# Optimization experiments

Hardware: AMD Instinct MI355X
Metric: run time of the kernel (lower is better)

Reference implementation:

```python
import jax, jax.numpy as jnp
import numpy as np

H, W, C = 512, 512, 21
D_BI, D_SP = 5, 2
THETA_ALPHA, THETA_BETA, THETA_GAMMA = 80.0, 13.0, 3.0
BILATERAL_COMPAT, SPATIAL_COMPAT, COMPAT = 10.0, 3.0, -1.0
NUM_ITER = 5


def _build_lattice(feats):
    # Permutohedral lattice construction (Adams et al. 2010), vectorized numpy.
    # feats: [N, d] float64 -> (offsets [N,d+1] int32 into M lattice points,
    # barycentric weights [N,d+1] float32, blur_neighbors [d+1, M, 2] int32 (+1, 0=missing)).
    N, d = feats.shape
    scale = (np.sqrt(2.0 / 3.0) * (d + 1)) / np.sqrt((np.arange(d) + 1.0) * (np.arange(d) + 2.0))
    cf = feats * scale                                            # [N, d]
    S = np.concatenate([np.cumsum(cf[:, ::-1], axis=1)[:, ::-1], np.zeros((N, 1))], axis=1)
    elev = np.empty((N, d + 1))
    elev[:, 0] = S[:, 0]
    elev[:, 1:] = S[:, 1:] - np.arange(1, d + 1) * cf             # embed on H_d hyperplane
    rem0 = np.floor(elev / (d + 1) + 0.5) * (d + 1)               # nearest 0-colored point
    sums = np.rint(rem0.sum(1) / (d + 1)).astype(np.int64)
    diff = elev - rem0
    idx = np.arange(d + 1)
    gt = diff[:, None, :] > diff[:, :, None]
    eq = (diff[:, None, :] == diff[:, :, None]) & (idx[None, None, :] < idx[None, :, None])
    rank = (gt | eq).sum(2).astype(np.int64) + sums[:, None]
    lo = rank < 0
    rank += (d + 1) * lo
    rem0 += (d + 1) * lo
    hi = rank > d
    rank -= (d + 1) * hi
    rem0 -= (d + 1) * hi
    v = (elev - rem0) / (d + 1)
    b = np.zeros((N, d + 2))
    rows = np.arange(N)[:, None]
    np.add.at(b, (rows, d - rank), v)
    np.add.at(b, (rows, d + 1 - rank), -v)
    b[:, 0] += 1.0 + b[:, d + 1]
    ws = b[:, :d + 1].astype(np.float32)                          # weight per remainder r
    rem0i = np.rint(rem0[:, :d]).astype(np.int64)
    r = np.arange(d + 1)
    keys = rem0i[:, None, :] + r[None, :, None] - (d + 1) * (rank[:, None, :d] > (d - r)[None, :, None])
    uniq, os_flat = np.unique(keys.reshape(-1, d), axis=0, return_inverse=True)
    M = uniq.shape[0]
    os_ = os_flat.reshape(N, d + 1).astype(np.int32)
    n1 = np.repeat(uniq[None] + 1, d + 1, axis=0)                 # [d+1, M, d]
    n2 = np.repeat(uniq[None] - 1, d + 1, axis=0)
    for j in range(d):
        n1[j, :, j] = uniq[:, j] - d
        n2[j, :, j] = uniq[:, j] + d
    allk = np.concatenate([uniq, n1.reshape(-1, d), n2.reshape(-1, d)], axis=0)
    _, inv = np.unique(allk, axis=0, return_inverse=True)
    lut = np.full(int(inv.max()) + 1, -1, np.int64)
    lut[inv[:M]] = np.arange(M)
    i1 = lut[inv[M:M + (d + 1) * M]].reshape(d + 1, M)
    i2 = lut[inv[M + (d + 1) * M:]].reshape(d + 1, M)
    bn = (np.stack([i1, i2], axis=-1) + 1).astype(np.int32)       # 0 == missing neighbor
    return os_, ws, bn


def setup_inputs():
    key = jax.random.key(0)
    k1, k2 = jax.random.split(key)
    unary = jax.random.normal(k1, (H, W, C), jnp.float32)
    # piecewise-constant random image (realistic local color coherence)
    base = np.asarray(jax.random.uniform(k2, (32, 32, 3)), dtype=np.float64) * 255.0
    image = np.kron(base, np.ones((H // 32, W // 32, 1)))
    yy, xx = np.mgrid[0:H, 0:W].astype(np.float64)
    bi = np.concatenate([np.stack([xx / THETA_ALPHA, yy / THETA_ALPHA], -1),
                         image / THETA_BETA], axis=-1).reshape(-1, D_BI)
    sp = np.stack([xx / THETA_GAMMA, yy / THETA_GAMMA], -1).reshape(-1, D_SP)
    os_b, ws_b, bn_b = _build_lattice(bi)
    os_s, ws_s, bn_s = _build_lattice(sp)
    return {'unary': unary,
            'ws_b': jnp.asarray(ws_b), 'ws_s': jnp.asarray(ws_s),
            'os_b': jnp.asarray(os_b), 'os_s': jnp.asarray(os_s),
            'bn_b': jnp.asarray(bn_b), 'bn_s': jnp.asarray(bn_s)}


def _filter(Q, os_, ws, bn, alpha):
    # splat -> blur -> slice over one permutohedral lattice
    M = bn.shape[1]
    vals = jnp.zeros((M + 1, Q.shape[-1]), Q.dtype)
    vals = vals.at[os_ + 1].add(ws[:, :, None] * Q[:, None, :])   # splat (row 0 = pad)
    for j in range(bn.shape[0]):                                  # blur along d+1 lattice axes
        vals = vals.at[1:].add(0.5 * (vals[bn[j, :, 0]] + vals[bn[j, :, 1]]))
    return alpha * jnp.einsum('nj,njc->nc', ws, vals[os_ + 1])    # slice


def reference(unary, ws_b, ws_s, os_b, os_s, bn_b, bn_s):
    U = unary.reshape(-1, unary.shape[-1])                        # [N, C]
    a_b = 1.0 / (1.0 + 2.0 ** (-D_BI))
    a_s = 1.0 / (1.0 + 2.0 ** (-D_SP))
    ones = jnp.ones((U.shape[0], 1), U.dtype)
    inv_nb = 1.0 / (_filter(ones, os_b, ws_b, bn_b, a_b) + 1e-20)
    inv_ns = 1.0 / (_filter(ones, os_s, ws_s, bn_s, a_s) + 1e-20)
    Q = jax.nn.softmax(-U, axis=-1)
    for _ in range(NUM_ITER):
        msg = BILATERAL_COMPAT * (_filter(Q, os_b, ws_b, bn_b, a_b) * inv_nb) \
            + SPATIAL_COMPAT * (_filter(Q, os_s, ws_s, bn_s, a_s) * inv_ns)
        Q = jax.nn.softmax(-U - COMPAT * msg, axis=-1)
    return Q.reshape(unary.shape)
```

## Files before the change

### kernel.cpp

```cpp
#include <hip/hip_runtime.h>
#include <hip/hip_fp16.h>

#define NCH 21
#define NCH2 22
#define VSH 32
#define QSH 32
#define USH 24
#define NPIX (512*512)
#define DECODE12 (1.0f/(4095.f*128.f))
#define DECODE14 (1.0f/(16383.f*128.f))

__device__ __forceinline__ float2 bits2f2(float b) {
  __half2 h = __builtin_bit_cast(__half2, b);
  return __half22float2(h);
}
__device__ __forceinline__ float f22bits(float x, float y) {
  __half2 h = __floats2half2_rn(x, y);
  return __builtin_bit_cast(float, h);
}

__device__ __forceinline__ int wave_rank_atomic(int m, bool valid, int* __restrict__ cur) {
  int lane = threadIdx.x & 63;
  unsigned long long todo = __ballot(valid);
  int out = 0;
  while (todo) {
    int leader = __ffsll((unsigned long long)todo) - 1;
    int lm = __shfl(m, leader);
    unsigned long long match = __ballot(valid && (m == lm));
    int cnt = __popcll(match);
    int b = 0;
    if (lane == leader) b = atomicAdd(&cur[lm], cnt);
    b = __shfl(b, leader);
    if (valid && (m == lm)) out = b + __popcll(match & ((1ull << lane) - 1ull));
    todo &= ~match;
  }
  return out;
}


__global__ void pack_count_kernel(const int* __restrict__ os_b, const float* __restrict__ ws_b,
                                  const int* __restrict__ os_s, const float* __restrict__ ws_s,
                                  unsigned int* __restrict__ sl, int* __restrict__ cnt,
                                  int nptot, int Mb) {
  int t = blockIdx.x*blockDim.x + threadIdx.x;
  bool valid = (t < nptot);
  int m = 0; float w = 0.f;
  if (valid) {
    if (t < 6*NPIX) { int j = t >> 18, n = t & (NPIX-1); m = os_b[n*6+j]; w = ws_b[n*6+j]; }
    else { int t2 = t - 6*NPIX; int j = t2 >> 18, n = t2 & (NPIX-1);
           m = Mb + os_s[n*3+j]; w = ws_s[n*3+j]; }
    int w12 = (int)(w * 4095.f + 0.5f);
    w12 = w12 < 0 ? 0 : (w12 > 4095 ? 4095 : w12);
    sl[t] = ((unsigned int)(m+1) << 12) | (unsigned int)w12;
  }
  int lane = threadIdx.x & 63;
  unsigned long long todo = __ballot(valid);
  while (todo) {
    int leader = __ffsll((unsigned long long)todo) - 1;
    int lm = __shfl(m, leader);
    unsigned long long match = __ballot(valid && (m == lm));
    if (lane == leader) atomicAdd(&cnt[lm], __popcll(match));
    todo &= ~match;
  }
}

__global__ void count_fused_kernel(const int* __restrict__ os_b, const int* __restrict__ os_s,
                                   int* __restrict__ cnt, int nptot, int Mb) {
  int t = blockIdx.x*blockDim.x + threadIdx.x;
  bool valid = (t < nptot);
  int m = 0;
  if (valid) {
    if (t < 6*NPIX) { int j = t >> 18, n = t & (NPIX-1); m = os_b[n*6+j]; }
    else { int t2 = t - 6*NPIX; int j = t2 >> 18, n = t2 & (NPIX-1); m = Mb + os_s[n*3+j]; }
  }
  int lane = threadIdx.x & 63;
  unsigned long long todo = __ballot(valid);
  while (todo) {
    int leader = __ffsll((unsigned long long)todo) - 1;
    int lm = __shfl(m, leader);
    unsigned long long match = __ballot(valid && (m == lm));
    if (lane == leader) atomicAdd(&cnt[lm], __popcll(match));
    todo &= ~match;
  }
}

__global__ void scan_block_kernel(const int* __restrict__ cnt, int* __restrict__ excl,
                                  int* __restrict__ bsum, int M) {
  __shared__ int s[256];
  int i = blockIdx.x*256 + threadIdx.x;
  int v = (i < M) ? cnt[i] : 0;
  s[threadIdx.x] = v;
  __syncthreads();
  for (int off = 1; off < 256; off <<= 1) {
    int t = (threadIdx.x >= off) ? s[threadIdx.x - off] : 0;
    __syncthreads();
    s[threadIdx.x] += t;
    __syncthreads();
  }
  if (i < M) excl[i] = s[threadIdx.x] - v;
  if (threadIdx.x == 255) bsum[blockIdx.x] = s[255];
}

__global__ void scan_sums_kernel(int* __restrict__ bsum, int nb) {
  __shared__ int s[256];
  __shared__ int carry;
  if (threadIdx.x == 0) carry = 0;
  __syncthreads();
  for (int base = 0; base < nb; base += 256) {
    int i = base + threadIdx.x;
    int v = (i < nb) ? bsum[i] : 0;
    s[threadIdx.x] = v;
    __syncthreads();
    for (int off = 1; off < 256; off <<= 1) {
      int t = (threadIdx.x >= off) ? s[threadIdx.x - off] : 0;
      __syncthreads();
      s[threadIdx.x] += t;
      __syncthreads();
    }
    if (i < nb) bsum[i] = s[threadIdx.x] - v + carry;
    int tot = s[255];
    __syncthreads();
    if (threadIdx.x == 0) carry += tot;
    __syncthreads();
  }
  if (threadIdx.x == 0) bsum[nb] = carry;
}

__global__ void scan_add_kernel(int* __restrict__ excl, const int* __restrict__ bsum,
                                int M, int nb) {
  int i = blockIdx.x*blockDim.x + threadIdx.x;
  if (i < M) excl[i] += bsum[i >> 8];
  else if (i == M) excl[M] = bsum[nb];
}

__global__ void fill_packed_kernel(const unsigned int* __restrict__ sl,
                                   const int* __restrict__ start, int* __restrict__ cur,
                                   unsigned int* __restrict__ pw, int nptot) {
  int t = blockIdx.x*blockDim.x + threadIdx.x;
  bool valid = (t < nptot);
  int m = 0; unsigned int e = 0;
  if (valid) {
    e = sl[t];
    m = (int)(e >> 12) - 1;
  }
  int slot = wave_rank_atomic(m, valid, cur);
  if (valid) {
    unsigned int pix = (unsigned int)(t & (NPIX-1));
    pw[start[m] + slot] = (pix << 12) | (e & 4095u);
  }
}

__global__ void fill_fused_kernel(const int* __restrict__ os_b, const float* __restrict__ ws_b,
                                  const int* __restrict__ os_s, const float* __restrict__ ws_s,
                                  const int* __restrict__ start, int* __restrict__ cur,
                                  unsigned int* __restrict__ pw, int nptot, int Mb) {
  int t = blockIdx.x*blockDim.x + threadIdx.x;
  bool valid = (t < nptot);
  int m = 0, pix = 0; float w = 0.f;
  if (valid) {
    if (t < 6*NPIX) { int j = t >> 18, n = t & (NPIX-1); m = os_b[n*6+j]; pix = n; w = ws_b[n*6+j]; }
    else { int t2 = t - 6*NPIX; int j = t2 >> 18, n = t2 & (NPIX-1);
           m = Mb + os_s[n*3+j]; pix = n; w = ws_s[n*3+j]; }
  }
  int slot = wave_rank_atomic(m, valid, cur);
  if (valid) {
    int w14 = (int)(w * 16383.f + 0.5f);
    w14 = w14 < 0 ? 0 : (w14 > 16383 ? 16383 : w14);
    pw[start[m] + slot] = ((unsigned int)pix << 14) | (unsigned int)w14;
  }
}


__global__ void gather_half2_kernel(const __half* __restrict__ Qh, const int* __restrict__ start,
                                    const unsigned int* __restrict__ pw,
                                    __half* __restrict__ valsB, __half* __restrict__ valsS,
                                    int Mb, int Mtot) {
  int wid = blockIdx.x*(blockDim.x >> 6) + (threadIdx.x >> 6);
  if (wid >= Mtot) return;
  int lane = threadIdx.x & 63;
  int pg = lane/11;
  int c2 = lane - pg*11;
  int k0 = start[wid], k1 = start[wid+1];
  float ax = 0.f, ay = 0.f, wsum = 0.f;
  if (pg < 5) {
    int k = k0 + pg;
    for (; k + 5 < k1; k += 10) {
      unsigned int e0 = pw[k], e1 = pw[k+5];
      float w0 = (float)(e0 & 4095u), w1 = (float)(e1 & 4095u);
      float2 f0 = __half22float2(*(const __half2*)(Qh + ((size_t)(e0 >> 12) << 5) + 2*c2));
      float2 f1 = __half22float2(*(const __half2*)(Qh + ((size_t)(e1 >> 12) << 5) + 2*c2));
      ax += w0*f0.x + w1*f1.x;
      ay += w0*f0.y + w1*f1.y;
      wsum += w0 + w1;
    }
    if (k < k1) {
      unsigned int e0 = pw[k];
      float w0 = (float)(e0 & 4095u);
      float2 f0 = __half22float2(*(const __half2*)(Qh + ((size_t)(e0 >> 12) << 5) + 2*c2));
      ax += w0*f0.x; ay += w0*f0.y; wsum += w0;
    }
  }
  float sx = ax, sy = ay, wt = wsum;
  #pragma unroll
  for (int g = 1; g < 5; ++g) {
    sx += __shfl(ax, lane + 11*g);
    sy += __shfl(ay, lane + 11*g);
    wt += __shfl(wsum, lane + 11*g);
  }
  if (lane < 11) {
    __half* row = (wid < Mb) ? (valsB + (size_t)(wid+1)*VSH)
                             : (valsS + (size_t)(wid-Mb+1)*VSH);
    float hy = (lane == 10) ? wt : sy;
    *(__half2*)(row + 2*lane) = __floats2half2_rn(sx*DECODE12, hy*DECODE12);
  }
}

__global__ void gather_wave_kernel(const __half* __restrict__ Qh, const int* __restrict__ start,
                                   const unsigned int* __restrict__ pw,
                                   __half* __restrict__ valsB, __half* __restrict__ valsS,
                                   int Mb, int Mtot) {
  const unsigned int WMASK = (1u << 14) - 1u;
  int wid = blockIdx.x*(blockDim.x >> 6) + (threadIdx.x >> 6);
  if (wid >= Mtot) return;
  int lane = threadIdx.x & 63;
  int pg = lane / 21;
  int c  = lane - pg*21;
  float s = 0.f, wsum = 0.f;
  int k1 = start[wid+1];
  if (pg < 3) {
    int k = start[wid] + pg;
    for (; k + 9 < k1; k += 12) {
      unsigned int a0 = pw[k], a1 = pw[k+3], a2 = pw[k+6], a3 = pw[k+9];
      float w0 = (float)(a0 & WMASK), w1 = (float)(a1 & WMASK);
      float w2 = (float)(a2 & WMASK), w3 = (float)(a3 & WMASK);
      s += w0 * __half2float(Qh[((size_t)(a0 >> 14) << 5) + c])
         + w1 * __half2float(Qh[((size_t)(a1 >> 14) << 5) + c])
         + w2 * __half2float(Qh[((size_t)(a2 >> 14) << 5) + c])
         + w3 * __half2float(Qh[((size_t)(a3 >> 14) << 5) + c]);
      wsum += w0 + w1 + w2 + w3;
    }
    for (; k < k1; k += 3) {
      unsigned int a = pw[k];
      float w = (float)(a & WMASK);
      s += w * __half2float(Qh[((size_t)(a >> 14) << 5) + c]);
      wsum += w;
    }
  }
  float s1 = __shfl(s, (lane + 21) & 63);
  float s2 = __shfl(s, (lane + 42) & 63);
  float wt = __shfl(wsum, 0) + __shfl(wsum, 21) + __shfl(wsum, 42);
  __half* row = (wid < Mb) ? (valsB + (size_t)(wid+1)*VSH)
                           : (valsS + (size_t)(wid-Mb+1)*VSH);
  if (lane < 21)       row[c]  = __float2half((s + s1 + s2) * DECODE14);
  else if (lane == 21) row[21] = __float2half(wt * DECODE14);
}

__global__ void blurH4_fused_kernel(const __half* __restrict__ inB, __half* __restrict__ outB,
                                    const int* __restrict__ bnB, int Mb,
                                    const __half* __restrict__ inS, __half* __restrict__ outS,
                                    const int* __restrict__ bnS, int Ms) {
  int t = blockIdx.x*blockDim.x + threadIdx.x;
  const __half* in; __half* out; const int* bn; int i, q;
  int tb = Mb*4;
  if (t < tb) { i = t>>2; q = t&3; in = inB; out = outB; bn = bnB; }
  else {
    int t2 = t - tb;
    if (t2 >= Ms*4) return;
    i = t2>>2; q = t2&3; in = inS; out = outS; bn = bnS;
  }
  int b0 = bn[2*i], b1 = bn[2*i+1];
  float4 A = ((const float4*)(in + (size_t)(i+1)*VSH))[q];
  float4 X = ((const float4*)(in + (size_t)b0*VSH))[q];
  float4 Y = ((const float4*)(in + (size_t)b1*VSH))[q];
  float4 O;
  const float* Af = (const float*)&A;
  const float* Xf = (const float*)&X;
  const float* Yf = (const float*)&Y;
  float* Of = (float*)&O;
  #pragma unroll
  for (int u = 0; u < 4; ++u) {
    float2 a = bits2f2(Af[u]);
    float2 x = bits2f2(Xf[u]);
    float2 y = bits2f2(Yf[u]);
    Of[u] = f22bits(a.x + 0.5f*(x.x + y.x), a.y + 0.5f*(x.y + y.y));
  }
  ((float4*)(out + (size_t)(i+1)*VSH))[q] = O;
}


__global__ void softmax_init_kernel(const float* __restrict__ U, __half* __restrict__ Qh,
                                    __half* __restrict__ Uh) {
  int n = blockIdx.x*blockDim.x + threadIdx.x;
  if (n >= NPIX) return;
  float l[NCH];
  float m = -3.4e38f;
  #pragma unroll
  for (int c = 0; c < NCH; ++c) {
    l[c] = -U[(size_t)n*NCH+c];
    m = fmaxf(m, l[c]);
  }
  {
    float buf[11];
    #pragma unroll
    for (int i = 0; i < 10; ++i) buf[i] = f22bits(l[2*i], l[2*i+1]);
    buf[10] = f22bits(l[20], 0.f);
    __half* u = Uh + (size_t)n*USH;
    *(float4*)(u)      = *(float4*)&buf[0];
    *(float4*)(u + 8)  = *(float4*)&buf[4];
    *(float2*)(u + 16) = *(float2*)&buf[8];
    *(float*)(u + 20)  = buf[10];
  }
  float s = 0.f;
  #pragma unroll
  for (int c = 0; c < NCH; ++c) { l[c] = expf(l[c]-m); s += l[c]; }
  float r = 1.0f/s;
  #pragma unroll
  for (int c = 0; c < NCH; ++c) l[c] *= r;
  {
    float buf[11];
    #pragma unroll
    for (int i = 0; i < 10; ++i) buf[i] = f22bits(l[2*i], l[2*i+1]);
    buf[10] = f22bits(l[20], 0.f);
    __half* q = Qh + (size_t)n*QSH;
    *(float4*)(q)      = *(float4*)&buf[0];
    *(float4*)(q + 8)  = *(float4*)&buf[4];
    *(float2*)(q + 16) = *(float2*)&buf[8];
    *(float*)(q + 20)  = buf[10];
  }
}

__device__ __forceinline__ void accum_row(const __half* __restrict__ v, float w, float2* acc2) {
  float4 a = *(const float4*)(v);
  float4 b = *(const float4*)(v + 8);
  float2 c = *(const float2*)(v + 16);
  float  d = *(const float*)(v + 20);
  float buf[11] = {a.x, a.y, a.z, a.w, b.x, b.y, b.z, b.w, c.x, c.y, d};
  #pragma unroll
  for (int i = 0; i < 11; ++i) {
    float2 f = bits2f2(buf[i]);
    acc2[i].x += w*f.x;
    acc2[i].y += w*f.y;
  }
}

template<bool FINAL, bool PACKED>
__global__ void slice_combine_softmax_kernel(
    const __half* __restrict__ Uh,
    const __half* __restrict__ vb, const __half* __restrict__ vsShift,
    const unsigned int* __restrict__ sl,
    const float* __restrict__ ws_b, const int* __restrict__ os_b,
    const float* __restrict__ ws_s, const int* __restrict__ os_s,
    float* __restrict__ QoutF, __half* __restrict__ QoutH) {
  int n = blockIdx.x*blockDim.x + threadIdx.x;
  if (n >= NPIX) return;
  float l[NCH];
  {
    const __half* u = Uh + (size_t)n*USH;
    float4 a = *(const float4*)(u);
    float4 b = *(const float4*)(u + 8);
    float2 c = *(const float2*)(u + 16);
    float buf[10] = {a.x, a.y, a.z, a.w, b.x, b.y, b.z, b.w, c.x, c.y};
    #pragma unroll
    for (int i = 0; i < 10; ++i) {
      float2 f = bits2f2(buf[i]);
      l[2*i] = f.x; l[2*i+1] = f.y;
    }
    l[20] = __half2float(u[20]);
  }
  float2 acc2[11];
  #pragma unroll
  for (int i = 0; i < 11; ++i) acc2[i] = make_float2(0.f, 0.f);
  #pragma unroll
  for (int j = 0; j < 6; ++j) {
    float w; const __half* v;
    if (PACKED) {
      unsigned int e = sl[(size_t)j*NPIX + n];
      w = (float)(e & 4095u);
      v = vb + ((size_t)(e >> 12) << 5);
    } else {
      w = ws_b[n*6+j];
      v = vb + (size_t)(os_b[n*6+j]+1)*VSH;
    }
    accum_row(v, w, acc2);
  }
  {
    float rb = 10.0f/(acc2[10].y + 1e-12f);
    #pragma unroll
    for (int i = 0; i < 10; ++i) { l[2*i] += rb*acc2[i].x; l[2*i+1] += rb*acc2[i].y; }
    l[20] += rb*acc2[10].x;
  }
  #pragma unroll
  for (int i = 0; i < 11; ++i) acc2[i] = make_float2(0.f, 0.f);
  #pragma unroll
  for (int j = 0; j < 3; ++j) {
    float w; const __half* v;
    if (PACKED) {
      unsigned int e = sl[(size_t)(6+j)*NPIX + n];
      w = (float)(e & 4095u);
      v = vsShift + ((size_t)(e >> 12) << 5);
    } else {
      w = ws_s[n*3+j];
      v = vsShift + (size_t)(os_s[n*3+j]+1)*VSH;
    }
    accum_row(v, w, acc2);
  }
  {
    float rs = 3.0f/(acc2[10].y + 1e-12f);
    #pragma unroll
    for (int i = 0; i < 10; ++i) { l[2*i] += rs*acc2[i].x; l[2*i+1] += rs*acc2[i].y; }
    l[20] += rs*acc2[10].x;
  }
  float m = -3.4e38f;
  #pragma unroll
  for (int c = 0; c < NCH; ++c) m = fmaxf(m, l[c]);
  float s = 0.f;
  #pragma unroll
  for (int c = 0; c < NCH; ++c) { l[c] = expf(l[c]-m); s += l[c]; }
  float r = 1.0f/s;
  if (FINAL) {
    #pragma unroll
    for (int c = 0; c < NCH; ++c) QoutF[(size_t)n*NCH+c] = l[c]*r;
  } else {
    float buf[11];
    #pragma unroll
    for (int i = 0; i < 10; ++i) buf[i] = f22bits(l[2*i]*r, l[2*i+1]*r);
    buf[10] = f22bits(l[20]*r, 0.f);
    __half* q = QoutH + (size_t)n*QSH;
    *(float4*)(q)      = *(float4*)&buf[0];
    *(float4*)(q + 8)  = *(float4*)&buf[4];
    *(float2*)(q + 16) = *(float2*)&buf[8];
    *(float*)(q + 20)  = buf[10];
  }
}


extern "C" void kernel_launch(void* const* d_in, const int* in_sizes, int n_in,
                              void* d_out, int out_size, void* d_ws, size_t ws_size,
                              hipStream_t stream) {
  const float* U    = (const float*)d_in[0];
  const float* ws_b = (const float*)d_in[1];
  const float* ws_s = (const float*)d_in[2];
  const int*   os_b = (const int*)d_in[3];
  const int*   os_s = (const int*)d_in[4];
  const int*   bn_b = (const int*)d_in[5];
  const int*   bn_s = (const int*)d_in[6];
  const int Mb = in_sizes[5] / 12;
  const int Ms = in_sizes[6] / 6;
  const int Mtot = Mb + Ms;
  const int nptot = NPIX*9;
  const bool packed = (Mtot + 1) < (1 << 20);

  char* wcur = (char*)d_ws;
  auto alloc = [&](size_t bytes) -> void* {
    void* p = (void*)wcur;
    wcur += (bytes + 63) & ~(size_t)63;
    return p;
  };
  __half* Qh     = (__half*)alloc((size_t)NPIX*QSH*2);
  __half* Uh     = (__half*)alloc((size_t)NPIX*USH*2);
  __half* vAb    = (__half*)alloc((size_t)(Mb+1)*VSH*2);
  __half* vBb    = (__half*)alloc((size_t)(Mb+1)*VSH*2);
  __half* vAs    = (__half*)alloc((size_t)(Ms+1)*VSH*2);
  __half* vBs    = (__half*)alloc((size_t)(Ms+1)*VSH*2);
  int*   start   = (int*)alloc((size_t)(Mtot+1)*4);
  int*   cur     = (int*)alloc((size_t)Mtot*4);
  unsigned int* pw = (unsigned int*)alloc((size_t)nptot*4);
  unsigned int* sl = (unsigned int*)alloc((size_t)nptot*4);
  int*   bsum    = (int*)alloc((size_t)(Mtot/256 + 3)*4);

  const int TB = 256;
  auto blocks = [](long long n){ return (int)((n + 255)/256); };
  const int nbM = blocks(Mtot);

  hipMemsetAsync(cur, 0, (size_t)Mtot*sizeof(int), stream);
  if (packed)
    pack_count_kernel<<<blocks(nptot), TB, 0, stream>>>(os_b, ws_b, os_s, ws_s,
                                                        sl, cur, nptot, Mb);
  else
    count_fused_kernel<<<blocks(nptot), TB, 0, stream>>>(os_b, os_s, cur, nptot, Mb);
  scan_block_kernel<<<nbM, 256, 0, stream>>>(cur, start, bsum, Mtot);
  scan_sums_kernel<<<1, 256, 0, stream>>>(bsum, nbM);
  scan_add_kernel<<<blocks(Mtot+1), TB, 0, stream>>>(start, bsum, Mtot, nbM);
  hipMemsetAsync(cur, 0, (size_t)Mtot*sizeof(int), stream);
  if (packed)
    fill_packed_kernel<<<blocks(nptot), TB, 0, stream>>>(sl, start, cur, pw, nptot);
  else
    fill_fused_kernel<<<blocks(nptot), TB, 0, stream>>>(os_b, ws_b, os_s, ws_s,
                                                        start, cur, pw, nptot, Mb);

  hipMemsetAsync(vAb, 0, VSH*2, stream);
  hipMemsetAsync(vBb, 0, VSH*2, stream);
  hipMemsetAsync(vAs, 0, VSH*2, stream);
  hipMemsetAsync(vBs, 0, VSH*2, stream);

  softmax_init_kernel<<<blocks(NPIX), TB, 0, stream>>>(U, Qh, Uh);

  for (int it = 0; it < 5; ++it) {
    if (packed)
      gather_half2_kernel<<<blocks((long long)Mtot*64), TB, 0, stream>>>(
          Qh, start, pw, vAb, vAs, Mb, Mtot);
    else
      gather_wave_kernel<<<blocks((long long)Mtot*64), TB, 0, stream>>>(
          Qh, start, pw, vAb, vAs, Mb, Mtot);
    __half* ab = vAb; __half* bb = vBb;
    __half* as = vAs; __half* bs = vBs;
    for (int j = 0; j < 6; ++j) {
      int ms = (j < 3) ? Ms : 0;
      blurH4_fused_kernel<<<blocks((long long)(Mb + ms)*4), TB, 0, stream>>>(
          ab, bb, bn_b + (size_t)j*Mb*2, Mb, as, bs, bn_s + (size_t)j*Ms*2, ms);
      { __half* t = ab; ab = bb; bb = t; }
      if (j < 3) { __half* t = as; as = bs; bs = t; }
    }
    const __half* vsArg = packed ? (as - (size_t)Mb*VSH) : as;
    if (it == 4) {
      if (packed)
        slice_combine_softmax_kernel<true,true><<<blocks(NPIX), TB, 0, stream>>>(
            Uh, ab, vsArg, sl, ws_b, os_b, ws_s, os_s, (float*)d_out, (__half*)nullptr);
      else
        slice_combine_softmax_kernel<true,false><<<blocks(NPIX), TB, 0, stream>>>(
            Uh, ab, vsArg, sl, ws_b, os_b, ws_s, os_s, (float*)d_out, (__half*)nullptr);
    } else {
      if (packed)
        slice_combine_softmax_kernel<false,true><<<blocks(NPIX), TB, 0, stream>>>(
            Uh, ab, vsArg, sl, ws_b, os_b, ws_s, os_s, (float*)nullptr, Qh);
      else
        slice_combine_softmax_kernel<false,false><<<blocks(NPIX), TB, 0, stream>>>(
            Uh, ab, vsArg, sl, ws_b, os_b, ws_s, os_s, (float*)nullptr, Qh);
    }
  }
}
```

Baseline: 483.1 us.

## Restructure pack-count per pixel, chunk gather loop, fold pad-row memsets into init

The packing/count kernel now runs one thread per pixel, loading all nine offsets and weights with vectorized reads and doing nine wave-aggregated atomic counts. The gather kernel splits each lattice point's entry list into contiguous chunks per lane group and reads packed entries with 8-byte loads, unrolled by four. The four small memsets that zero the pad rows are moved into the softmax init kernel, removing separate launches. Per-pixel counting may see less atomic aggregation within a wave, and the contiguous chunking changes the memory access pattern in the hot gather.

```diff
diff --git a/kernel.cpp b/kernel.cpp
--- a/kernel.cpp
+++ b/kernel.cpp
@@ -37,30 +37,53 @@
   return out;
 }
 
-
-__global__ void pack_count_kernel(const int* __restrict__ os_b, const float* __restrict__ ws_b,
-                                  const int* __restrict__ os_s, const float* __restrict__ ws_s,
-                                  unsigned int* __restrict__ sl, int* __restrict__ cnt,
-                                  int nptot, int Mb) {
-  int t = blockIdx.x*blockDim.x + threadIdx.x;
-  bool valid = (t < nptot);
-  int m = 0; float w = 0.f;
-  if (valid) {
-    if (t < 6*NPIX) { int j = t >> 18, n = t & (NPIX-1); m = os_b[n*6+j]; w = ws_b[n*6+j]; }
-    else { int t2 = t - 6*NPIX; int j = t2 >> 18, n = t2 & (NPIX-1);
-           m = Mb + os_s[n*3+j]; w = ws_s[n*3+j]; }
-    int w12 = (int)(w * 4095.f + 0.5f);
-    w12 = w12 < 0 ? 0 : (w12 > 4095 ? 4095 : w12);
-    sl[t] = ((unsigned int)(m+1) << 12) | (unsigned int)w12;
-  }
+__device__ __forceinline__ void wave_count_atomic(int m, int* __restrict__ cnt) {
   int lane = threadIdx.x & 63;
-  unsigned long long todo = __ballot(valid);
+  unsigned long long todo = ~0ull;
   while (todo) {
     int leader = __ffsll((unsigned long long)todo) - 1;
     int lm = __shfl(m, leader);
-    unsigned long long match = __ballot(valid && (m == lm));
-    if (lane == leader) atomicAdd(&cnt[lm], __popcll(match));
+    unsigned long long match = __ballot(m == lm);
+    if (lane == leader) atomicAdd(&cnt[lm], __popcll(match & todo));
     todo &= ~match;
+  }
+}
+
+
+__global__ void pack9_count_kernel(const int* __restrict__ os_b, const float* __restrict__ ws_b,
+                                   const int* __restrict__ os_s, const float* __restrict__ ws_s,
+                                   unsigned int* __restrict__ sl, int* __restrict__ cnt,
+                                   int Mb) {
+  int n = blockIdx.x*blockDim.x + threadIdx.x;
+  if (n >= NPIX) return;
+  int ob[6]; float wb[6];
+  {
+    const int2* p = (const int2*)(os_b + (size_t)n*6);
+    int2 a = p[0], b = p[1], c = p[2];
+    ob[0]=a.x; ob[1]=a.y; ob[2]=b.x; ob[3]=b.y; ob[4]=c.x; ob[5]=c.y;
+    const float2* q = (const float2*)(ws_b + (size_t)n*6);
+    float2 d = q[0], e = q[1], f = q[2];
+    wb[0]=d.x; wb[1]=d.y; wb[2]=e.x; wb[3]=e.y; wb[4]=f.x; wb[5]=f.y;
+  }
+  int osv[3]; float wsv[3];
+  #pragma unroll
+  for (int j = 0; j < 3; ++j) { osv[j] = os_s[(size_t)n*3+j]; wsv[j] = ws_s[(size_t)n*3+j]; }
+
+  #pragma unroll
+  for (int j = 0; j < 6; ++j) {
+    int m = ob[j];
+    int w12 = (int)(wb[j] * 4095.f + 0.5f);
+    w12 = w12 < 0 ? 0 : (w12 > 4095 ? 4095 : w12);
+    sl[(size_t)j*NPIX + n] = ((unsigned int)(m+1) << 12) | (unsigned int)w12;
+    wave_count_atomic(m, cnt);
+  }
+  #pragma unroll
+  for (int j = 0; j < 3; ++j) {
+    int m = Mb + osv[j];
+    int w12 = (int)(wsv[j] * 4095.f + 0.5f);
+    w12 = w12 < 0 ? 0 : (w12 > 4095 ? 4095 : w12);
+    sl[(size_t)(6+j)*NPIX + n] = ((unsigned int)(m+1) << 12) | (unsigned int)w12;
+    wave_count_atomic(m, cnt);
   }
 }
 
@@ -183,17 +206,32 @@
   int k0 = start[wid], k1 = start[wid+1];
   float ax = 0.f, ay = 0.f, wsum = 0.f;
   if (pg < 5) {
-    int k = k0 + pg;
-    for (; k + 5 < k1; k += 10) {
-      unsigned int e0 = pw[k], e1 = pw[k+5];
-      float w0 = (float)(e0 & 4095u), w1 = (float)(e1 & 4095u);
+    int len = k1 - k0;
+    int L = (len + 4) / 5;
+    int ka = k0 + pg*L;
+    int kb = ka + L; if (kb > k1) kb = k1;
+    int k = ka;
+    if (k < kb && (k & 1)) {
+      unsigned int e0 = pw[k];
+      float w0 = (float)(e0 & 4095u);
       float2 f0 = __half22float2(*(const __half2*)(Qh + ((size_t)(e0 >> 12) << 5) + 2*c2));
-      float2 f1 = __half22float2(*(const __half2*)(Qh + ((size_t)(e1 >> 12) << 5) + 2*c2));
-      ax += w0*f0.x + w1*f1.x;
-      ay += w0*f0.y + w1*f1.y;
-      wsum += w0 + w1;
-    }
-    if (k < k1) {
+      ax += w0*f0.x; ay += w0*f0.y; wsum += w0;
+      ++k;
+    }
+    for (; k + 3 < kb; k += 4) {
+      uint2 ea = *(const uint2*)(pw + k);
+      uint2 eb = *(const uint2*)(pw + k + 2);
+      float w0 = (float)(ea.x & 4095u), w1 = (float)(ea.y & 4095u);
+      float w2 = (float)(eb.x & 4095u), w3 = (float)(eb.y & 4095u);
+      float2 f0 = __half22float2(*(const __half2*)(Qh + ((size_t)(ea.x >> 12) << 5) + 2*c2));
+      float2 f1 = __half22float2(*(const __half2*)(Qh + ((size_t)(ea.y >> 12) << 5) + 2*c2));
+      float2 f2 = __half22float2(*(const __half2*)(Qh + ((size_t)(eb.x >> 12) << 5) + 2*c2));
+      float2 f3 = __half22float2(*(const __half2*)(Qh + ((size_t)(eb.y >> 12) << 5) + 2*c2));
+      ax += w0*f0.x + w1*f1.x + w2*f2.x + w3*f3.x;
+      ay += w0*f0.y + w1*f1.y + w2*f2.y + w3*f3.y;
+      wsum += w0 + w1 + w2 + w3;
+    }
+    for (; k < kb; ++k) {
       unsigned int e0 = pw[k];
       float w0 = (float)(e0 & 4095u);
       float2 f0 = __half22float2(*(const __half2*)(Qh + ((size_t)(e0 >> 12) << 5) + 2*c2));
@@ -289,8 +327,15 @@
 
 
 __global__ void softmax_init_kernel(const float* __restrict__ U, __half* __restrict__ Qh,
-                                    __half* __restrict__ Uh) {
+                                    __half* __restrict__ Uh,
+                                    __half* __restrict__ vAb, __half* __restrict__ vBb,
+                                    __half* __restrict__ vAs, __half* __restrict__ vBs) {
   int n = blockIdx.x*blockDim.x + threadIdx.x;
+  if (blockIdx.x == 0 && threadIdx.x < 64) {
+    int t = threadIdx.x & 15;
+    __half* rows[4] = {vAb, vBb, vAs, vBs};
+    ((float*)rows[threadIdx.x >> 4])[t] = 0.f;
+  }
   if (n >= NPIX) return;
   float l[NCH];
   float m = -3.4e38f;
@@ -474,8 +519,8 @@
 
   hipMemsetAsync(cur, 0, (size_t)Mtot*sizeof(int), stream);
   if (packed)
-    pack_count_kernel<<<blocks(nptot), TB, 0, stream>>>(os_b, ws_b, os_s, ws_s,
-                                                        sl, cur, nptot, Mb);
+    pack9_count_kernel<<<blocks(NPIX), TB, 0, stream>>>(os_b, ws_b, os_s, ws_s,
+                                                        sl, cur, Mb);
   else
     count_fused_kernel<<<blocks(nptot), TB, 0, stream>>>(os_b, os_s, cur, nptot, Mb);
   scan_block_kernel<<<nbM, 256, 0, stream>>>(cur, start, bsum, Mtot);
@@ -488,12 +533,7 @@
     fill_fused_kernel<<<blocks(nptot), TB, 0, stream>>>(os_b, ws_b, os_s, ws_s,
                                                         start, cur, pw, nptot, Mb);
 
-  hipMemsetAsync(vAb, 0, VSH*2, stream);
-  hipMemsetAsync(vBb, 0, VSH*2, stream);
-  hipMemsetAsync(vAs, 0, VSH*2, stream);
-  hipMemsetAsync(vBs, 0, VSH*2, stream);
-
-  softmax_init_kernel<<<blocks(NPIX), TB, 0, stream>>>(U, Qh, Uh);
+  softmax_init_kernel<<<blocks(NPIX), TB, 0, stream>>>(U, Qh, Uh, vAb, vBb, vAs, vBs);
 
   for (int it = 0; it < 5; ++it) {
     if (packed)
```

New measurement: 452.6 us (median of 2 runs). 6.3% less time.
